# Kernel optimization log

Hardware: AMD Instinct MI355X
Metric: run time of the kernel (lower is better)

The kernel has to match this reference:

```python
import jax, jax.numpy as jnp
import numpy as np
from jax import lax

B_, L_, D_, N_, K_ = 2, 4096, 1024, 16, 4


def setup_inputs() -> dict:
    key = jax.random.key(0)
    ks = jax.random.split(key, 11)
    s = lambda fan: 1.0 / np.sqrt(fan)
    return {
        "x": jax.random.normal(ks[0], (B_, L_, D_), jnp.float32),
        "W_in": jax.random.normal(ks[1], (D_, 2 * D_), jnp.float32) * s(D_),
        "b_in": jax.random.normal(ks[2], (2 * D_,), jnp.float32) * 0.01,
        "conv_w": jax.random.normal(ks[3], (D_, K_), jnp.float32) * s(K_),
        "conv_b": jax.random.normal(ks[4], (D_,), jnp.float32) * 0.01,
        "W_x": jax.random.normal(ks[5], (D_, 2 * N_), jnp.float32) * s(D_),
        "b_x": jax.random.normal(ks[6], (2 * N_,), jnp.float32) * 0.01,
        "A_log": jax.random.normal(ks[7], (D_, N_), jnp.float32),
        "D_param": jnp.ones((D_,), jnp.float32),
        "W_out": jax.random.normal(ks[8], (D_, D_), jnp.float32) * s(D_),
        "b_out": jax.random.normal(ks[9], (D_,), jnp.float32) * 0.01,
    }


def silu(x):
    return x * jax.nn.sigmoid(x)


def s6_forward(x, W_in, b_in, conv_w, conv_b, W_x, b_x, A_log, D_param, W_out, b_out):
    b, L, D = x.shape
    # in_proj then split into ssm stream and gate
    x_and_gate = x @ W_in + b_in                      # [b, L, 2D]
    x_ssm, gate = jnp.split(x_and_gate, 2, axis=-1)   # each [b, L, D]

    # depthwise causal conv: padding=(d_conv-1, d_conv-1) then [:, :, :L] == left-pad only
    xc = jnp.transpose(x_ssm, (0, 2, 1))              # [b, D, L]
    xc = lax.conv_general_dilated(
        xc, conv_w[:, None, :],                       # [D, 1, K]
        window_strides=(1,), padding=[(K_ - 1, 0)],
        feature_group_count=D,
        dimension_numbers=("NCH", "OIH", "NCH"),
    ) + conv_b[None, :, None]
    x_conv = silu(jnp.transpose(xc, (0, 2, 1)))       # [b, L, D]

    # data-dependent B, C
    BC = x_conv @ W_x + b_x                           # [b, L, 2N]
    B_mat, C_mat = jnp.split(BC, 2, axis=-1)          # each [b, L, N]

    A_discrete = jnp.exp(-jnp.exp(A_log))             # [D, N]

    # sequential selective scan over L, carry h: [b, D, N]
    def step(h, inp):
        xc_t, B_t, C_t = inp                          # [b,D], [b,N], [b,N]
        h = A_discrete[None] * h + xc_t[:, :, None] * B_t[:, None, :]
        y = jnp.einsum("bn,bdn->bd", C_t, h) + D_param * xc_t
        return h, y

    h0 = jnp.zeros((b, D, N_), x.dtype)
    xs = (jnp.transpose(x_conv, (1, 0, 2)),
          jnp.transpose(B_mat, (1, 0, 2)),
          jnp.transpose(C_mat, (1, 0, 2)))
    h_final, ys = lax.scan(step, h0, xs)              # ys: [L, b, D]
    y = jnp.transpose(ys, (1, 0, 2))                  # [b, L, D]

    y = y * silu(gate)
    y = y @ W_out + b_out
    final_state = h_final.mean(axis=1)                # [b, N]
    return y, final_state


def reference(x, W_in, b_in, conv_w, conv_b, W_x, b_x, A_log, D_param, W_out, b_out):
    return s6_forward(x, W_in, b_in, conv_w, conv_b, W_x, b_x, A_log, D_param, W_out, b_out)
```

## Files before the change

kernel.cpp:

```cpp
#include <hip/hip_runtime.h>
#include <hip/hip_bf16.h>
#include <math.h>

#define LL 4096
#define DD 1024
#define NN 16
#define KK 4
#define BB 2
#define MM (BB * LL)
#define NC 64
#define LC 64

typedef unsigned short ushort_t;
typedef short s16x8 __attribute__((ext_vector_type(8)));
typedef float f32x4 __attribute__((ext_vector_type(4)));
typedef unsigned int u32;

__device__ __forceinline__ ushort_t f2bf(float f) {
  __hip_bfloat16 h = __float2bfloat16(f);
  return *reinterpret_cast<ushort_t*>(&h);
}
__device__ __forceinline__ float bf2f(ushort_t u) {
  union { u32 i; float f; } c;
  c.i = ((u32)u) << 16;
  return c.f;
}

template <bool BF16OUT>
__global__ __launch_bounds__(256) void gemm_bt_mfma(
    const ushort_t* __restrict__ A,
    const ushort_t* __restrict__ BT,
    const float* __restrict__ bias,
    void* __restrict__ Cv, int N) {
  constexpr int K = 1024;
  __shared__ ushort_t As[128 * 64];
  __shared__ ushort_t Bs[128 * 64];

  const int tid = threadIdx.x;
  const int lane = tid & 63;
  const int w = tid >> 6;
  const int wm = w & 1, wn = w >> 1;
  const int row0 = blockIdx.y * 128;
  const int col0 = blockIdx.x * 128;

  const int lrow8 = lane >> 3;
  const int lkc = (lane & 7) ^ lrow8;

  f32x4 acc[4][4];
#pragma unroll
  for (int i = 0; i < 4; ++i)
#pragma unroll
    for (int j = 0; j < 4; ++j) acc[i][j] = (f32x4){0.f, 0.f, 0.f, 0.f};

  const int frow = lane & 15;
  const int quad = lane >> 4;
  const int r7 = frow & 7;

  for (int k0 = 0; k0 < K; k0 += 64) {
#pragma unroll
    for (int it = 0; it < 4; ++it) {
      int r = it * 32 + w * 8;
      __builtin_amdgcn_global_load_lds(
          (const __attribute__((address_space(1))) u32*)(A + (size_t)(row0 + r + lrow8) * K + k0 + lkc * 8),
          (__attribute__((address_space(3))) u32*)(As + r * 64), 16, 0, 0);
      __builtin_amdgcn_global_load_lds(
          (const __attribute__((address_space(1))) u32*)(BT + (size_t)(col0 + r + lrow8) * K + k0 + lkc * 8),
          (__attribute__((address_space(3))) u32*)(Bs + r * 64), 16, 0, 0);
    }
    __syncthreads();

#pragma unroll
    for (int half = 0; half < 2; ++half) {
      s16x8 af[4], bf[4];
#pragma unroll
      for (int mi = 0; mi < 4; ++mi)
        af[mi] = *(const s16x8*)&As[(wm * 64 + mi * 16 + frow) * 64 +
                                    (((half * 4 + quad) ^ r7) * 8)];
#pragma unroll
      for (int ni = 0; ni < 4; ++ni)
        bf[ni] = *(const s16x8*)&Bs[(wn * 64 + ni * 16 + frow) * 64 +
                                    (((half * 4 + quad) ^ r7) * 8)];
#pragma unroll
      for (int mi = 0; mi < 4; ++mi)
#pragma unroll
        for (int ni = 0; ni < 4; ++ni)
          acc[mi][ni] = __builtin_amdgcn_mfma_f32_16x16x32_bf16(
              af[mi], bf[ni], acc[mi][ni], 0, 0, 0);
    }
    __syncthreads();
  }

#pragma unroll
  for (int mi = 0; mi < 4; ++mi) {
#pragma unroll
    for (int ni = 0; ni < 4; ++ni) {
      int col = col0 + wn * 64 + ni * 16 + frow;
      float b = bias[col];
#pragma unroll
      for (int r = 0; r < 4; ++r) {
        int row = row0 + wm * 64 + mi * 16 + quad * 4 + r;
        if constexpr (BF16OUT)
          ((ushort_t*)Cv)[(size_t)row * N + col] = f2bf(acc[mi][ni][r] + b);
        else
          ((float*)Cv)[(size_t)row * N + col] = acc[mi][ni][r] + b;
      }
    }
  }
}

__global__ __launch_bounds__(128) void bc_mfma_k(
    const ushort_t* __restrict__ A,
    const ushort_t* __restrict__ BT,
    const float* __restrict__ bias,
    float* __restrict__ C) {
  constexpr int K = 1024;
  __shared__ ushort_t As[32 * 32];
  __shared__ ushort_t Bs[32 * 32];

  const int tid = threadIdx.x;
  const int lane = tid & 63;
  const int w = tid >> 6;
  const int row0 = blockIdx.x * 32;
  const int lrow = lane >> 2;
  const int lkc = (lane & 3) ^ ((lrow >> 1) & 3);
  const int frow = lane & 15;
  const int quad = lane >> 4;
  const int sw = (frow >> 1) & 3;

  f32x4 acc[2];
  acc[0] = (f32x4){0.f, 0.f, 0.f, 0.f};
  acc[1] = (f32x4){0.f, 0.f, 0.f, 0.f};

  for (int k0 = 0; k0 < K; k0 += 32) {
    __builtin_amdgcn_global_load_lds(
        (const __attribute__((address_space(1))) u32*)(A + (size_t)(row0 + w * 16 + lrow) * K + k0 + lkc * 8),
        (__attribute__((address_space(3))) u32*)(As + (w * 16) * 32), 16, 0, 0);
    __builtin_amdgcn_global_load_lds(
        (const __attribute__((address_space(1))) u32*)(BT + (size_t)(w * 16 + lrow) * K + k0 + lkc * 8),
        (__attribute__((address_space(3))) u32*)(Bs + (w * 16) * 32), 16, 0, 0);
    __syncthreads();

    s16x8 af = *(const s16x8*)&As[(w * 16 + frow) * 32 + (quad ^ sw) * 8];
    s16x8 bf0 = *(const s16x8*)&Bs[(frow)*32 + (quad ^ sw) * 8];
    s16x8 bf1 = *(const s16x8*)&Bs[(16 + frow) * 32 + (quad ^ sw) * 8];
    acc[0] = __builtin_amdgcn_mfma_f32_16x16x32_bf16(af, bf0, acc[0], 0, 0, 0);
    acc[1] = __builtin_amdgcn_mfma_f32_16x16x32_bf16(af, bf1, acc[1], 0, 0, 0);
    __syncthreads();
  }

#pragma unroll
  for (int ni = 0; ni < 2; ++ni) {
    int col = ni * 16 + frow;
    float b = bias[col];
#pragma unroll
    for (int r = 0; r < 4; ++r) {
      int row = row0 + w * 16 + quad * 4 + r;
      C[(size_t)row * 32 + col] = acc[ni][r] + b;
    }
  }
}

__global__ __launch_bounds__(256) void prep_k(
    const float* __restrict__ x, ushort_t* __restrict__ Xb,
    float* __restrict__ fs, const float* __restrict__ W_in,
    const float* __restrict__ W_out, const float* __restrict__ W_x,
    ushort_t* __restrict__ WinT, ushort_t* __restrict__ WoutT,
    ushort_t* __restrict__ WxT) {
  constexpr int K = 1024;
  const int tid = threadIdx.x;
  if (blockIdx.z == 0) {
    if (blockIdx.x == 0 && blockIdx.y == 0 && tid < 32) fs[tid] = 0.f;
    int i = (blockIdx.y * 64 + blockIdx.x) * 256 + tid;
    float4 v = ((const float4*)x)[i];
    ushort4 o;
    o.x = f2bf(v.x); o.y = f2bf(v.y); o.z = f2bf(v.z); o.w = f2bf(v.w);
    ((ushort4*)Xb)[i] = o;
    return;
  }
  const float* W;
  ushort_t* WT;
  int N;
  int by = blockIdx.y;
  if (by < 32) {
    W = W_in; WT = WinT; N = 2048;
  } else if (by < 64) {
    if (blockIdx.x >= 32) return;
    W = W_out; WT = WoutT; N = 1024;
    by -= 32;
  } else if (by < 96) {
    if (blockIdx.x >= 1) return;
    W = W_x; WT = WxT; N = 32;
    by -= 64;
  } else {
    return;
  }
  __shared__ float t[32][33];
  int nb = blockIdx.x * 32, kb = by * 32;
  int tx = tid & 31, ty = tid >> 5;
#pragma unroll
  for (int i = 0; i < 32; i += 8)
    t[ty + i][tx] = W[(size_t)(kb + ty + i) * N + nb + tx];
  __syncthreads();
#pragma unroll
  for (int i = 0; i < 32; i += 8)
    WT[(size_t)(nb + ty + i) * K + kb + tx] = f2bf(t[tx][ty + i]);
}

__global__ __launch_bounds__(256) void conv_silu_k(
    const ushort_t* __restrict__ XGb, const float* __restrict__ conv_w,
    const float* __restrict__ conv_b, ushort_t* __restrict__ XCb) {
  __shared__ float cw[128 * 33];
  const int tid = threadIdx.x;
#pragma unroll
  for (int j = 0; j < 4; ++j) {
    int d = tid + j * 256;
    float4 v = ((const float4*)conv_w)[d];
    float* p = &cw[(d >> 3) * 33 + (d & 7) * 4];
    p[0] = v.x; p[1] = v.y; p[2] = v.z; p[3] = v.w;
  }
  __syncthreads();

  int gid = blockIdx.x * 256 + tid;
  int m = gid >> 7;
  int dg = gid & 127;
  int d0 = dg * 8;
  int l = m & (LL - 1);
  const float* w = &cw[dg * 33];

  float4 b0 = ((const float4*)conv_b)[dg * 2];
  float4 b1 = ((const float4*)conv_b)[dg * 2 + 1];
  float acc[8] = {b0.x, b0.y, b0.z, b0.w, b1.x, b1.y, b1.z, b1.w};

#pragma unroll
  for (int k = 0; k < KK; ++k) {
    int li = l + k - (KK - 1);
    if (li < 0) continue;
    s16x8 v = *(const s16x8*)(XGb + (size_t)(m + k - (KK - 1)) * 2048 + d0);
#pragma unroll
    for (int j = 0; j < 8; ++j)
      acc[j] += bf2f((ushort_t)v[j]) * w[j * 4 + k];
  }
  ushort_t o[8];
#pragma unroll
  for (int j = 0; j < 8; ++j) {
    float s = acc[j] / (1.f + __expf(-acc[j]));
    o[j] = f2bf(s);
  }
  *(s16x8*)(XCb + (size_t)m * DD + d0) = *(const s16x8*)o;
}

__global__ __launch_bounds__(64) void scan_local_k(
    const ushort_t* __restrict__ XCb, const float* __restrict__ BC,
    const float* __restrict__ A_log, float* __restrict__ S) {
  const int b = blockIdx.x, c = blockIdx.y;
  const int tid = threadIdx.x;
  const int d0 = blockIdx.z * 128 + tid * 2;
  const int t0 = c * LC;
  const size_t rowb = (size_t)b * LL;

  __shared__ float bcs[LC * 32];
  {
    const float4* src = (const float4*)(BC + (rowb + t0) * 32);
    float4* dst = (float4*)bcs;
#pragma unroll
    for (int i = 0; i < 8; ++i) dst[tid + i * 64] = src[tid + i * 64];
  }

  float a0[NN], a1[NN], h0[NN], h1[NN];
#pragma unroll
  for (int n = 0; n < NN; ++n) {
    a0[n] = expf(-expf(A_log[d0 * NN + n]));
    a1[n] = expf(-expf(A_log[(d0 + 1) * NN + n]));
    h0[n] = 0.f;
    h1[n] = 0.f;
  }
  __syncthreads();

  const ushort_t* xp = XCb + (rowb + t0) * DD + d0;
  u32 xw = *(const u32*)xp;
  for (int t = 0; t < LC; ++t) {
    u32 xw_n = (t + 1 < LC) ? *(const u32*)(xp + (size_t)(t + 1) * DD) : 0u;
    float x0 = bf2f((ushort_t)(xw & 0xffff));
    float x1 = bf2f((ushort_t)(xw >> 16));
    const float* bp = bcs + t * 32;
#pragma unroll
    for (int n = 0; n < NN; ++n) {
      float bv = bp[n];
      h0[n] = a0[n] * h0[n] + x0 * bv;
      h1[n] = a1[n] * h1[n] + x1 * bv;
    }
    xw = xw_n;
  }
  float* sp = S + (((size_t)(b * NC + c)) * DD + d0) * NN;
#pragma unroll
  for (int n = 0; n < NN; ++n) sp[n] = h0[n];
#pragma unroll
  for (int n = 0; n < NN; ++n) sp[NN + n] = h1[n];
}

__global__ __launch_bounds__(256) void scan_carry_k(
    float* __restrict__ S, const float* __restrict__ A_log,
    float* __restrict__ fs) {
  const int idx = blockIdx.x * 256 + threadIdx.x;
  const int n = idx & (NN - 1);
  const int d = (idx / NN) & (DD - 1);
  const int b = idx / (NN * DD);

  const float aLC = expf(-(float)LC * expf(A_log[d * NN + n]));
  float h = 0.f;
  for (int c = 0; c < NC; ++c) {
    size_t off = (((size_t)(b * NC + c)) * DD + d) * NN + n;
    float s = S[off];
    S[off] = h;
    h = aLC * h + s;
  }
  __shared__ float red[256];
  red[threadIdx.x] = h * (1.f / (float)DD);
  __syncthreads();
  if (threadIdx.x < NN) {
    float sum = 0.f;
#pragma unroll
    for (int i = 0; i < 16; ++i) sum += red[i * NN + threadIdx.x];
    atomicAdd(&fs[b * NN + threadIdx.x], sum);
  }
}

__global__ __launch_bounds__(64) void scan_final_k(
    const ushort_t* __restrict__ XCb, const ushort_t* __restrict__ XGb,
    const float* __restrict__ BC, const float* __restrict__ A_log,
    const float* __restrict__ D_param, const float* __restrict__ H0,
    ushort_t* __restrict__ Y1b) {
  const int b = blockIdx.x, c = blockIdx.y;
  const int tid = threadIdx.x;
  const int d0 = blockIdx.z * 128 + tid * 2;
  const int t0 = c * LC;
  const size_t rowb = (size_t)b * LL;

  __shared__ float bcs[LC * 32];
  {
    const float4* src = (const float4*)(BC + (rowb + t0) * 32);
    float4* dst = (float4*)bcs;
#pragma unroll
    for (int i = 0; i < 8; ++i) dst[tid + i * 64] = src[tid + i * 64];
  }

  float a0[NN], a1[NN], h0[NN], h1[NN];
  const float* hp = H0 + (((size_t)(b * NC + c)) * DD + d0) * NN;
#pragma unroll
  for (int n = 0; n < NN; ++n) {
    a0[n] = expf(-expf(A_log[d0 * NN + n]));
    a1[n] = expf(-expf(A_log[(d0 + 1) * NN + n]));
    h0[n] = hp[n];
    h1[n] = hp[NN + n];
  }
  const float Dp0 = D_param[d0], Dp1 = D_param[d0 + 1];
  __syncthreads();

  const ushort_t* xp = XCb + (rowb + t0) * DD + d0;
  const ushort_t* gp = XGb + (rowb + t0) * 2048 + DD + d0;
  ushort_t* yp = Y1b + (rowb + t0) * DD + d0;
  u32 xw = *(const u32*)xp;
  u32 gw = *(const u32*)gp;
  for (int t = 0; t < LC; ++t) {
    u32 xw_n = 0u, gw_n = 0u;
    if (t + 1 < LC) {
      xw_n = *(const u32*)(xp + (size_t)(t + 1) * DD);
      gw_n = *(const u32*)(gp + (size_t)(t + 1) * 2048);
    }
    float x0 = bf2f((ushort_t)(xw & 0xffff));
    float x1 = bf2f((ushort_t)(xw >> 16));
    float g0 = bf2f((ushort_t)(gw & 0xffff));
    float g1 = bf2f((ushort_t)(gw >> 16));
    float y0 = Dp0 * x0, y1 = Dp1 * x1;
    const float* bp = bcs + t * 32;
#pragma unroll
    for (int n = 0; n < NN; ++n) {
      float bv = bp[n], cv = bp[16 + n];
      h0[n] = a0[n] * h0[n] + x0 * bv;
      h1[n] = a1[n] * h1[n] + x1 * bv;
      y0 += cv * h0[n];
      y1 += cv * h1[n];
    }
    float sg0 = g0 / (1.f + __expf(-g0));
    float sg1 = g1 / (1.f + __expf(-g1));
    u32 outw = (u32)f2bf(y0 * sg0) | ((u32)f2bf(y1 * sg1) << 16);
    *(u32*)(yp + (size_t)t * DD) = outw;
    xw = xw_n;
    gw = gw_n;
  }
}

extern "C" void kernel_launch(void* const* d_in, const int* in_sizes, int n_in,
                              void* d_out, int out_size, void* d_ws,
                              size_t ws_size, hipStream_t stream) {
  const float* x = (const float*)d_in[0];
  const float* W_in = (const float*)d_in[1];
  const float* b_in = (const float*)d_in[2];
  const float* conv_w = (const float*)d_in[3];
  const float* conv_b = (const float*)d_in[4];
  const float* W_x = (const float*)d_in[5];
  const float* b_x = (const float*)d_in[6];
  const float* A_log = (const float*)d_in[7];
  const float* D_param = (const float*)d_in[8];
  const float* W_out = (const float*)d_in[9];
  const float* b_out = (const float*)d_in[10];
  float* out = (float*)d_out;
  float* fs = out + (size_t)MM * DD;

  float* BC = (float*)d_ws;
  float* S = BC + (size_t)MM * 32;
  ushort_t* Xb = (ushort_t*)(S + (size_t)BB * NC * DD * NN);
  ushort_t* XGb = Xb + (size_t)MM * DD;
  ushort_t* XCb = XGb + (size_t)MM * 2048;
  ushort_t* Y1b = XCb + (size_t)MM * DD;
  ushort_t* WinT = Y1b + (size_t)MM * DD;
  ushort_t* WoutT = WinT + (size_t)2048 * DD;
  ushort_t* WxT = WoutT + (size_t)DD * DD;

  dim3 blk(256);
  prep_k<<<dim3(64, 128, 2), blk, 0, stream>>>(x, Xb, fs, W_in, W_out, W_x,
                                               WinT, WoutT, WxT);
  gemm_bt_mfma<true><<<dim3(2048 / 128, MM / 128), blk, 0, stream>>>(
      Xb, WinT, b_in, XGb, 2048);
  conv_silu_k<<<dim3((MM * 128) / 256), blk, 0, stream>>>(XGb, conv_w, conv_b,
                                                          XCb);
  bc_mfma_k<<<dim3(MM / 32), dim3(128), 0, stream>>>(XCb, WxT, b_x, BC);
  scan_local_k<<<dim3(BB, NC, DD / 128), dim3(64), 0, stream>>>(XCb, BC, A_log,
                                                                S);
  scan_carry_k<<<dim3((BB * DD * NN) / 256), blk, 0, stream>>>(S, A_log, fs);
  scan_final_k<<<dim3(BB, NC, DD / 128), dim3(64), 0, stream>>>(
      XCb, XGb, BC, A_log, D_param, S, Y1b);
  gemm_bt_mfma<false><<<dim3(1024 / 128, MM / 128), blk, 0, stream>>>(
      Y1b, WoutT, b_out, out, 1024);
}
```

Measured before the change: 270.7 us.

## Halve scan chunk length, pack 4 chunks per block, precompute decay, transpose state layout

```diff
diff --git a/kernel.cpp b/kernel.cpp
--- a/kernel.cpp
+++ b/kernel.cpp
@@ -8,8 +8,8 @@
 #define KK 4
 #define BB 2
 #define MM (BB * LL)
-#define NC 64
-#define LC 64
+#define NC 128
+#define LC 32
 
 typedef unsigned short ushort_t;
 typedef short s16x8 __attribute__((ext_vector_type(8)));
@@ -109,10 +109,8 @@
 }
 
 __global__ __launch_bounds__(128) void bc_mfma_k(
-    const ushort_t* __restrict__ A,
-    const ushort_t* __restrict__ BT,
-    const float* __restrict__ bias,
-    float* __restrict__ C) {
+    const ushort_t* __restrict__ A, const ushort_t* __restrict__ BT,
+    const float* __restrict__ bias, float* __restrict__ C) {
   constexpr int K = 1024;
   __shared__ ushort_t As[32 * 32];
   __shared__ ushort_t Bs[32 * 32];
@@ -165,7 +163,8 @@
     float* __restrict__ fs, const float* __restrict__ W_in,
     const float* __restrict__ W_out, const float* __restrict__ W_x,
     ushort_t* __restrict__ WinT, ushort_t* __restrict__ WoutT,
-    ushort_t* __restrict__ WxT) {
+    ushort_t* __restrict__ WxT, const float* __restrict__ A_log,
+    float* __restrict__ Adis, float* __restrict__ ALC) {
   constexpr int K = 1024;
   const int tid = threadIdx.x;
   if (blockIdx.z == 0) {
@@ -177,22 +176,31 @@
     ((ushort4*)Xb)[i] = o;
     return;
   }
+  int by = blockIdx.y;
+  if (by >= 96) {
+    if (by >= 104 || blockIdx.x != 0) return;
+    int base = (by - 96) * 2048 + tid * 8;
+#pragma unroll
+    for (int j = 0; j < 8; ++j) {
+      float e = __expf(A_log[base + j]);
+      Adis[base + j] = __expf(-e);
+      ALC[base + j] = __expf(-(float)LC * e);
+    }
+    return;
+  }
   const float* W;
   ushort_t* WT;
   int N;
-  int by = blockIdx.y;
   if (by < 32) {
     W = W_in; WT = WinT; N = 2048;
   } else if (by < 64) {
     if (blockIdx.x >= 32) return;
     W = W_out; WT = WoutT; N = 1024;
     by -= 32;
-  } else if (by < 96) {
+  } else {
     if (blockIdx.x >= 1) return;
     W = W_x; WT = WxT; N = 32;
     by -= 64;
-  } else {
-    return;
   }
   __shared__ float t[32][33];
   int nb = blockIdx.x * 32, kb = by * 32;
@@ -249,32 +257,32 @@
   *(s16x8*)(XCb + (size_t)m * DD + d0) = *(const s16x8*)o;
 }
 
-__global__ __launch_bounds__(64) void scan_local_k(
+__global__ __launch_bounds__(256) void scan_local_k(
     const ushort_t* __restrict__ XCb, const float* __restrict__ BC,
-    const float* __restrict__ A_log, float* __restrict__ S) {
-  const int b = blockIdx.x, c = blockIdx.y;
-  const int tid = threadIdx.x;
-  const int d0 = blockIdx.z * 128 + tid * 2;
+    const float* __restrict__ Adis, float* __restrict__ S) {
+  const int b = blockIdx.x;
+  const int w = threadIdx.x >> 6;
+  const int lane = threadIdx.x & 63;
+  const int c = blockIdx.y * 4 + w;
+  const int d0 = blockIdx.z * 128 + lane * 2;
   const int t0 = c * LC;
   const size_t rowb = (size_t)b * LL;
 
-  __shared__ float bcs[LC * 32];
+  __shared__ float bcs_all[4][LC * 32];
+  float* bcs = bcs_all[w];
   {
     const float4* src = (const float4*)(BC + (rowb + t0) * 32);
     float4* dst = (float4*)bcs;
 #pragma unroll
-    for (int i = 0; i < 8; ++i) dst[tid + i * 64] = src[tid + i * 64];
-  }
-
-  float a0[NN], a1[NN], h0[NN], h1[NN];
-#pragma unroll
-  for (int n = 0; n < NN; ++n) {
-    a0[n] = expf(-expf(A_log[d0 * NN + n]));
-    a1[n] = expf(-expf(A_log[(d0 + 1) * NN + n]));
-    h0[n] = 0.f;
-    h1[n] = 0.f;
-  }
-  __syncthreads();
+    for (int i = 0; i < 4; ++i) dst[lane + i * 64] = src[lane + i * 64];
+  }
+  f32x4 av[8];
+#pragma unroll
+  for (int i = 0; i < 8; ++i) av[i] = *(const f32x4*)(Adis + d0 * 16 + i * 4);
+
+  float h0[NN], h1[NN];
+#pragma unroll
+  for (int n = 0; n < NN; ++n) { h0[n] = 0.f; h1[n] = 0.f; }
 
   const ushort_t* xp = XCb + (rowb + t0) * DD + d0;
   u32 xw = *(const u32*)xp;
@@ -286,75 +294,80 @@
 #pragma unroll
     for (int n = 0; n < NN; ++n) {
       float bv = bp[n];
-      h0[n] = a0[n] * h0[n] + x0 * bv;
-      h1[n] = a1[n] * h1[n] + x1 * bv;
+      h0[n] = av[n >> 2][n & 3] * h0[n] + x0 * bv;
+      h1[n] = av[4 + (n >> 2)][n & 3] * h1[n] + x1 * bv;
     }
     xw = xw_n;
   }
-  float* sp = S + (((size_t)(b * NC + c)) * DD + d0) * NN;
-#pragma unroll
-  for (int n = 0; n < NN; ++n) sp[n] = h0[n];
-#pragma unroll
-  for (int n = 0; n < NN; ++n) sp[NN + n] = h1[n];
+  float* sp = S + ((size_t)(b * NC + c) * NN) * DD + d0;
+#pragma unroll
+  for (int n = 0; n < NN; ++n) {
+    float2 v = {h0[n], h1[n]};
+    *(float2*)(sp + (size_t)n * DD) = v;
+  }
 }
 
 __global__ __launch_bounds__(256) void scan_carry_k(
-    float* __restrict__ S, const float* __restrict__ A_log,
+    float* __restrict__ S, const float* __restrict__ ALC,
     float* __restrict__ fs) {
   const int idx = blockIdx.x * 256 + threadIdx.x;
-  const int n = idx & (NN - 1);
-  const int d = (idx / NN) & (DD - 1);
-  const int b = idx / (NN * DD);
-
-  const float aLC = expf(-(float)LC * expf(A_log[d * NN + n]));
+  const int d = idx & (DD - 1);
+  const int n = (idx >> 10) & (NN - 1);
+  const int b = idx >> 14;
+
+  const float aLC = ALC[d * NN + n];
   float h = 0.f;
   for (int c = 0; c < NC; ++c) {
-    size_t off = (((size_t)(b * NC + c)) * DD + d) * NN + n;
+    size_t off = ((size_t)(b * NC + c) * NN + n) * DD + d;
     float s = S[off];
     S[off] = h;
     h = aLC * h + s;
   }
   __shared__ float red[256];
-  red[threadIdx.x] = h * (1.f / (float)DD);
+  red[threadIdx.x] = h;
   __syncthreads();
-  if (threadIdx.x < NN) {
-    float sum = 0.f;
-#pragma unroll
-    for (int i = 0; i < 16; ++i) sum += red[i * NN + threadIdx.x];
-    atomicAdd(&fs[b * NN + threadIdx.x], sum);
-  }
-}
-
-__global__ __launch_bounds__(64) void scan_final_k(
+#pragma unroll
+  for (int s2 = 128; s2 > 0; s2 >>= 1) {
+    if (threadIdx.x < s2) red[threadIdx.x] += red[threadIdx.x + s2];
+    __syncthreads();
+  }
+  if (threadIdx.x == 0) atomicAdd(&fs[b * NN + n], red[0] * (1.f / (float)DD));
+}
+
+__global__ __launch_bounds__(256) void scan_final_k(
     const ushort_t* __restrict__ XCb, const ushort_t* __restrict__ XGb,
-    const float* __restrict__ BC, const float* __restrict__ A_log,
+    const float* __restrict__ BC, const float* __restrict__ Adis,
     const float* __restrict__ D_param, const float* __restrict__ H0,
     ushort_t* __restrict__ Y1b) {
-  const int b = blockIdx.x, c = blockIdx.y;
-  const int tid = threadIdx.x;
-  const int d0 = blockIdx.z * 128 + tid * 2;
+  const int b = blockIdx.x;
+  const int w = threadIdx.x >> 6;
+  const int lane = threadIdx.x & 63;
+  const int c = blockIdx.y * 4 + w;
+  const int d0 = blockIdx.z * 128 + lane * 2;
   const int t0 = c * LC;
   const size_t rowb = (size_t)b * LL;
 
-  __shared__ float bcs[LC * 32];
+  __shared__ float bcs_all[4][LC * 32];
+  float* bcs = bcs_all[w];
   {
     const float4* src = (const float4*)(BC + (rowb + t0) * 32);
     float4* dst = (float4*)bcs;
 #pragma unroll
-    for (int i = 0; i < 8; ++i) dst[tid + i * 64] = src[tid + i * 64];
-  }
-
-  float a0[NN], a1[NN], h0[NN], h1[NN];
-  const float* hp = H0 + (((size_t)(b * NC + c)) * DD + d0) * NN;
+    for (int i = 0; i < 4; ++i) dst[lane + i * 64] = src[lane + i * 64];
+  }
+  f32x4 av[8];
+#pragma unroll
+  for (int i = 0; i < 8; ++i) av[i] = *(const f32x4*)(Adis + d0 * 16 + i * 4);
+
+  float h0[NN], h1[NN];
+  const float* hp = H0 + ((size_t)(b * NC + c) * NN) * DD + d0;
 #pragma unroll
   for (int n = 0; n < NN; ++n) {
-    a0[n] = expf(-expf(A_log[d0 * NN + n]));
-    a1[n] = expf(-expf(A_log[(d0 + 1) * NN + n]));
-    h0[n] = hp[n];
-    h1[n] = hp[NN + n];
-  }
-  const float Dp0 = D_param[d0], Dp1 = D_param[d0 + 1];
-  __syncthreads();
+    float2 v = *(const float2*)(hp + (size_t)n * DD);
+    h0[n] = v.x;
+    h1[n] = v.y;
+  }
+  float2 Dp = *(const float2*)(D_param + d0);
 
   const ushort_t* xp = XCb + (rowb + t0) * DD + d0;
   const ushort_t* gp = XGb + (rowb + t0) * 2048 + DD + d0;
@@ -371,13 +384,13 @@
     float x1 = bf2f((ushort_t)(xw >> 16));
     float g0 = bf2f((ushort_t)(gw & 0xffff));
     float g1 = bf2f((ushort_t)(gw >> 16));
-    float y0 = Dp0 * x0, y1 = Dp1 * x1;
+    float y0 = Dp.x * x0, y1 = Dp.y * x1;
     const float* bp = bcs + t * 32;
 #pragma unroll
     for (int n = 0; n < NN; ++n) {
       float bv = bp[n], cv = bp[16 + n];
-      h0[n] = a0[n] * h0[n] + x0 * bv;
-      h1[n] = a1[n] * h1[n] + x1 * bv;
+      h0[n] = av[n >> 2][n & 3] * h0[n] + x0 * bv;
+      h1[n] = av[4 + (n >> 2)][n & 3] * h1[n] + x1 * bv;
       y0 += cv * h0[n];
       y1 += cv * h1[n];
     }
@@ -409,7 +422,9 @@
 
   float* BC = (float*)d_ws;
   float* S = BC + (size_t)MM * 32;
-  ushort_t* Xb = (ushort_t*)(S + (size_t)BB * NC * DD * NN);
+  float* Adis = S + (size_t)BB * NC * NN * DD;
+  float* ALC = Adis + (size_t)DD * NN;
+  ushort_t* Xb = (ushort_t*)(ALC + (size_t)DD * NN);
   ushort_t* XGb = Xb + (size_t)MM * DD;
   ushort_t* XCb = XGb + (size_t)MM * 2048;
   ushort_t* Y1b = XCb + (size_t)MM * DD;
@@ -419,17 +434,18 @@
 
   dim3 blk(256);
   prep_k<<<dim3(64, 128, 2), blk, 0, stream>>>(x, Xb, fs, W_in, W_out, W_x,
-                                               WinT, WoutT, WxT);
+                                               WinT, WoutT, WxT, A_log, Adis,
+                                               ALC);
   gemm_bt_mfma<true><<<dim3(2048 / 128, MM / 128), blk, 0, stream>>>(
       Xb, WinT, b_in, XGb, 2048);
   conv_silu_k<<<dim3((MM * 128) / 256), blk, 0, stream>>>(XGb, conv_w, conv_b,
                                                           XCb);
   bc_mfma_k<<<dim3(MM / 32), dim3(128), 0, stream>>>(XCb, WxT, b_x, BC);
-  scan_local_k<<<dim3(BB, NC, DD / 128), dim3(64), 0, stream>>>(XCb, BC, A_log,
-                                                                S);
-  scan_carry_k<<<dim3((BB * DD * NN) / 256), blk, 0, stream>>>(S, A_log, fs);
-  scan_final_k<<<dim3(BB, NC, DD / 128), dim3(64), 0, stream>>>(
-      XCb, XGb, BC, A_log, D_param, S, Y1b);
+  scan_local_k<<<dim3(BB, NC / 4, DD / 128), blk, 0, stream>>>(XCb, BC, Adis,
+                                                               S);
+  scan_carry_k<<<dim3((BB * DD * NN) / 256), blk, 0, stream>>>(S, ALC, fs);
+  scan_final_k<<<dim3(BB, NC / 4, DD / 128), blk, 0, stream>>>(
+      XCb, XGb, BC, Adis, D_param, S, Y1b);
   gemm_bt_mfma<false><<<dim3(1024 / 128, MM / 128), blk, 0, stream>>>(
       Y1b, WoutT, b_out, out, 1024);
 }
```

New measurement: 249.7 us. 7.8% less time.
